# Optimization experiments

Measured on AMD Instinct MI355X. Metric: run time of the kernel, lower is better.

The kernel has to match this reference:

```python
import jax, jax.numpy as jnp
import numpy as np


def setup_inputs() -> dict:
    key = jax.random.key(0)
    B, C, H, W = 32, 128, 112, 112
    inp = jax.random.normal(key, (B, C, H, W), dtype=jnp.float32)
    # binomial blur filter for filt_size=4: outer([1,3,3,1]) normalized, repeated per channel
    a = np.array([1.0, 3.0, 3.0, 1.0])
    f = a[:, None] * a[None, :]
    f = f / f.sum()
    filt = jnp.asarray(np.broadcast_to(f[None, None], (C, 1, 4, 4)).copy(), dtype=jnp.float32)
    return {"inp": inp, "filt": filt}


def _polyphase_select_l2(x):
    # x: [B,C,H,W] with even H,W (aps_pad is a no-op). Returns [B] int index in {0..3}.
    p0 = x[:, :, 0::2, 0::2]
    p1 = x[:, :, 1::2, 0::2]
    p2 = x[:, :, 0::2, 1::2]
    p3 = x[:, :, 1::2, 1::2]
    norms = jnp.stack(
        [jnp.sqrt(jnp.sum(p * p, axis=(1, 2, 3))) for p in (p0, p1, p2, p3)], axis=1
    )  # [B,4]
    return jnp.argmax(norms, axis=1)


def reference(inp, filt):
    # 1) per-sample polyphase component selection on the raw input (criterion 'l2')
    idx = _polyphase_select_l2(inp)  # [B]
    C = inp.shape[1]
    # 2) reflect pad (left=1, right=2, top=1, bottom=2 for filt_size=4) + depthwise blur
    xp = jnp.pad(inp, ((0, 0), (0, 0), (1, 2), (1, 2)), mode='reflect')
    blurred = jax.lax.conv_general_dilated(
        xp, filt, window_strides=(1, 1), padding='VALID',
        dimension_numbers=('NCHW', 'OIHW', 'NCHW'), feature_group_count=C)
    # 3) stride-2 polyphase downsample selecting the chosen phase per sample
    p0 = blurred[:, :, 0::2, 0::2]
    p1 = blurred[:, :, 1::2, 0::2]
    p2 = blurred[:, :, 0::2, 1::2]
    p3 = blurred[:, :, 1::2, 1::2]
    poly = jnp.stack([p0, p1, p2, p3], axis=1)  # [B,4,C,H/2,W/2]
    out = jnp.take_along_axis(poly, idx[:, None, None, None, None], axis=1)[:, 0]
    return out  # [B,C,H/2,W/2]
```

## Files before the change

kernel.cpp:

```cpp
#include <hip/hip_runtime.h>

#define HW_    12544
#define W_     112
#define C_     128
#define OHW_   3136
#define OW_    56
#define NCHUNK 49

__global__ __launch_bounds__(512) void phase_norms(const float* __restrict__ inp,
                                                   float* __restrict__ part) {
    const int b = blockIdx.y;
    const float4* src = (const float4*)(inp + (size_t)b * (C_ * HW_));
    const unsigned tid = threadIdx.x;
    const unsigned base = blockIdx.x * 8192u + tid;

    float s[4] = {0.f, 0.f, 0.f, 0.f};
#pragma unroll
    for (int k = 0; k < 16; ++k) {
        unsigned g = base + k * 512u;
        float4 v = src[g];
        unsigned hp = (g / 28u) & 1u;
        s[hp]      += v.x * v.x + v.z * v.z;
        s[hp + 2u] += v.y * v.y + v.w * v.w;
    }

#pragma unroll
    for (int p = 0; p < 4; ++p) {
        float v = s[p];
        for (int off = 32; off > 0; off >>= 1) v += __shfl_down(v, off);
        s[p] = v;
    }

    __shared__ float bs[8][4];
    const unsigned wid = tid >> 6;
    if ((tid & 63u) == 0u) {
#pragma unroll
        for (int p = 0; p < 4; ++p) bs[wid][p] = s[p];
    }
    __syncthreads();
    if (tid < 4) {
        float v = 0.f;
#pragma unroll
        for (int w = 0; w < 8; ++w) v += bs[w][tid];
        part[((size_t)b * NCHUNK + blockIdx.x) * 4 + tid] = v;
    }
}

__global__ __launch_bounds__(128) void finalize_idx(const float* __restrict__ part,
                                                    int* __restrict__ pidx) {
    const int t = threadIdx.x;
    const int b = t >> 2, p = t & 3;
    float s = 0.f;
    for (int c = 0; c < NCHUNK; ++c) s += part[b * (NCHUNK * 4) + c * 4 + p];
    const int g = t & ~3;
    const float v0 = __shfl(s, g + 0), v1 = __shfl(s, g + 1);
    const float v2 = __shfl(s, g + 2), v3 = __shfl(s, g + 3);
    if (p == 0) {
        int idx = 0; float best = v0;
        if (v1 > best) { best = v1; idx = 1; }
        if (v2 > best) { best = v2; idx = 2; }
        if (v3 > best) { best = v3; idx = 3; }
        pidx[b] = idx;
    }
}

__global__ __launch_bounds__(256) void blur_select(const float* __restrict__ inp,
                                                   const int* __restrict__ pidx,
                                                   float* __restrict__ out) {
    __shared__ float h[59 * 56];
    const int blk = blockIdx.x;
    const int bc  = blk >> 1;
    const int oh0 = (blk & 1) * 28;
    const int t   = threadIdx.x;

    const int phase = pidx[bc >> 7];
    const int dr = phase & 1, dc = phase >> 1;
    const float* P = inp + (size_t)bc * HW_;
    const int jbase = 2 * oh0 - 1;

    for (int q = t; q < 59 * 5; q += 256) {
        const int rr = q / 5;
        const int s  = 1 + (q - 5 * rr);
        int j = jbase + rr;
        int aj = j < 0 ? -j : j;
        j = aj < 222 - aj ? aj : 222 - aj;
        const float4* rp = (const float4*)(P + j * W_) + (4 * s - 1);
        float4 va[6];
#pragma unroll
        for (int i = 0; i < 6; ++i) va[i] = rp[i];
        float xa[24];
#pragma unroll
        for (int i = 0; i < 6; ++i) {
            xa[4 * i + 0] = va[i].x; xa[4 * i + 1] = va[i].y;
            xa[4 * i + 2] = va[i].z; xa[4 * i + 3] = va[i].w;
        }
        float hh[8];
        if (dc == 0) {
#pragma unroll
            for (int u = 0; u < 8; ++u)
                hh[u] = (xa[2*u+3] + xa[2*u+6]) + 3.f * (xa[2*u+4] + xa[2*u+5]);
        } else {
#pragma unroll
            for (int u = 0; u < 8; ++u)
                hh[u] = (xa[2*u+4] + xa[2*u+7]) + 3.f * (xa[2*u+5] + xa[2*u+6]);
        }
        float* dst = &h[rr * 56 + 8 * s];
        *(float4*)dst       = make_float4(hh[0], hh[1], hh[2], hh[3]);
        *(float4*)(dst + 4) = make_float4(hh[4], hh[5], hh[6], hh[7]);
    }

    for (int rr = t; rr < 59; rr += 256) {
        int j = jbase + rr;
        int aj = j < 0 ? -j : j;
        j = aj < 222 - aj ? aj : 222 - aj;
        const float4* rp = (const float4*)(P + j * W_);
        float4 a4[5], b4[5];
#pragma unroll
        for (int i = 0; i < 5; ++i) { a4[i] = rp[i]; b4[i] = rp[23 + i]; }
        float xa[20], xb[22];
#pragma unroll
        for (int i = 0; i < 5; ++i) {
            xa[4*i+0] = a4[i].x; xa[4*i+1] = a4[i].y; xa[4*i+2] = a4[i].z; xa[4*i+3] = a4[i].w;
            xb[4*i+0] = b4[i].x; xb[4*i+1] = b4[i].y; xb[4*i+2] = b4[i].z; xb[4*i+3] = b4[i].w;
        }
        xb[20] = xb[18];
        xb[21] = xb[17];
        float hl[8], hr[8];
        if (dc == 0) {
            hl[0] = (xa[1] + xa[2]) + 3.f * (xa[0] + xa[1]);
#pragma unroll
            for (int u = 1; u < 8; ++u)
                hl[u] = (xa[2*u-1] + xa[2*u+2]) + 3.f * (xa[2*u] + xa[2*u+1]);
#pragma unroll
            for (int u = 0; u < 8; ++u)
                hr[u] = (xb[2*u+3] + xb[2*u+6]) + 3.f * (xb[2*u+4] + xb[2*u+5]);
        } else {
#pragma unroll
            for (int u = 0; u < 8; ++u)
                hl[u] = (xa[2*u] + xa[2*u+3]) + 3.f * (xa[2*u+1] + xa[2*u+2]);
#pragma unroll
            for (int u = 0; u < 8; ++u)
                hr[u] = (xb[2*u+4] + xb[2*u+7]) + 3.f * (xb[2*u+5] + xb[2*u+6]);
        }
        float* dl = &h[rr * 56];
        *(float4*)dl        = make_float4(hl[0], hl[1], hl[2], hl[3]);
        *(float4*)(dl + 4)  = make_float4(hl[4], hl[5], hl[6], hl[7]);
        *(float4*)(dl + 48) = make_float4(hr[0], hr[1], hr[2], hr[3]);
        *(float4*)(dl + 52) = make_float4(hr[4], hr[5], hr[6], hr[7]);
    }

    __syncthreads();

    float* o = out + (size_t)bc * OHW_ + oh0 * OW_;
    for (int v = t; v < 392; v += 256) {
        const int ohl = v / 14;
        const int q   = v - 14 * ohl;
        const float* hb = &h[(2 * ohl + dr) * 56 + 4 * q];
        const float4 h0 = *(const float4*)hb;
        const float4 h1 = *(const float4*)(hb + 56);
        const float4 h2 = *(const float4*)(hb + 112);
        const float4 h3 = *(const float4*)(hb + 168);
        float4 r;
        r.x = ((h0.x + h3.x) + 3.f * (h1.x + h2.x)) * 0.015625f;
        r.y = ((h0.y + h3.y) + 3.f * (h1.y + h2.y)) * 0.015625f;
        r.z = ((h0.z + h3.z) + 3.f * (h1.z + h2.z)) * 0.015625f;
        r.w = ((h0.w + h3.w) + 3.f * (h1.w + h2.w)) * 0.015625f;
        *(float4*)&o[ohl * 56 + 4 * q] = r;
    }
}

extern "C" void kernel_launch(void* const* d_in, const int* in_sizes, int n_in,
                              void* d_out, int out_size, void* d_ws, size_t ws_size,
                              hipStream_t stream) {
    const float* inp = (const float*)d_in[0];
    float* part = (float*)d_ws;
    int* pidx = (int*)((char*)d_ws + 32 * NCHUNK * 4 * sizeof(float));
    phase_norms<<<dim3(NCHUNK, 32), 512, 0, stream>>>(inp, part);
    finalize_idx<<<1, 128, 0, stream>>>(part, pidx);
    blur_select<<<8192, 256, 0, stream>>>(inp, pidx, (float*)d_out);
}
```

Before: 88.72 us.

## Compute blur outputs directly per thread without shared-memory staging

Replaces the shared-memory horizontal-pass staging in blur_select with a per-thread direct computation. Each thread reads four reflected input rows of 24 floats and produces 8 outputs, with no __syncthreads. It also computes only the rows needed for the selected row phase, rather than every row of the tile. This removes LDS traffic and the block barrier, at the cost of redundant global/L2 reads of overlapping input rows across threads. The grid is resized so each thread owns one 8-wide output segment.

```diff
diff --git a/kernel.cpp b/kernel.cpp
--- a/kernel.cpp
+++ b/kernel.cpp
@@ -23,14 +23,12 @@
         s[hp]      += v.x * v.x + v.z * v.z;
         s[hp + 2u] += v.y * v.y + v.w * v.w;
     }
-
 #pragma unroll
     for (int p = 0; p < 4; ++p) {
         float v = s[p];
         for (int off = 32; off > 0; off >>= 1) v += __shfl_down(v, off);
         s[p] = v;
     }
-
     __shared__ float bs[8][4];
     const unsigned wid = tid >> 6;
     if ((tid & 63u) == 0u) {
@@ -67,106 +65,75 @@
 __global__ __launch_bounds__(256) void blur_select(const float* __restrict__ inp,
                                                    const int* __restrict__ pidx,
                                                    float* __restrict__ out) {
-    __shared__ float h[59 * 56];
-    const int blk = blockIdx.x;
-    const int bc  = blk >> 1;
-    const int oh0 = (blk & 1) * 28;
-    const int t   = threadIdx.x;
+    const int g  = blockIdx.x * 256 + threadIdx.x;
+    const int bc = g / 392;
+    const int r  = g - bc * 392;
+    const int oh = r / 7;
+    const int s  = r - oh * 7;
+    const int ph = pidx[bc >> 7];
+    const int dr = ph & 1, dc = ph >> 1;
+    const float* P = inp + (size_t)bc * HW_;
 
-    const int phase = pidx[bc >> 7];
-    const int dr = phase & 1, dc = phase >> 1;
-    const float* P = inp + (size_t)bc * HW_;
-    const int jbase = 2 * oh0 - 1;
+    const int base4 = (s == 0) ? 0 : ((s == 6) ? 22 : 4 * s - 1);
+    const int jb = 2 * oh + dr - 1;
 
-    for (int q = t; q < 59 * 5; q += 256) {
-        const int rr = q / 5;
-        const int s  = 1 + (q - 5 * rr);
-        int j = jbase + rr;
+    float acc[8] = {0.f, 0.f, 0.f, 0.f, 0.f, 0.f, 0.f, 0.f};
+
+#pragma unroll
+    for (int k = 0; k < 4; ++k) {
+        int j = jb + k;
         int aj = j < 0 ? -j : j;
         j = aj < 222 - aj ? aj : 222 - aj;
-        const float4* rp = (const float4*)(P + j * W_) + (4 * s - 1);
-        float4 va[6];
+        const float4* rp = (const float4*)(P + j * W_) + base4;
+        const float4 v0 = rp[0], v1 = rp[1], v2 = rp[2];
+        const float4 v3 = rp[3], v4 = rp[4], v5 = rp[5];
+        float y[24] = {v0.x, v0.y, v0.z, v0.w, v1.x, v1.y, v1.z, v1.w,
+                       v2.x, v2.y, v2.z, v2.w, v3.x, v3.y, v3.z, v3.w,
+                       v4.x, v4.y, v4.z, v4.w, v5.x, v5.y, v5.z, v5.w};
+        float h[8];
+        if (s == 0) {
+            if (dc == 0) {
+                h[0] = 3.f * y[0] + 4.f * y[1] + y[2];
 #pragma unroll
-        for (int i = 0; i < 6; ++i) va[i] = rp[i];
-        float xa[24];
+                for (int u = 1; u < 8; ++u)
+                    h[u] = (y[2*u-1] + y[2*u+2]) + 3.f * (y[2*u] + y[2*u+1]);
+            } else {
 #pragma unroll
-        for (int i = 0; i < 6; ++i) {
-            xa[4 * i + 0] = va[i].x; xa[4 * i + 1] = va[i].y;
-            xa[4 * i + 2] = va[i].z; xa[4 * i + 3] = va[i].w;
+                for (int u = 0; u < 8; ++u)
+                    h[u] = (y[2*u] + y[2*u+3]) + 3.f * (y[2*u+1] + y[2*u+2]);
+            }
+        } else if (s == 6) {
+            if (dc == 0) {
+#pragma unroll
+                for (int u = 0; u < 7; ++u)
+                    h[u] = (y[2*u+7] + y[2*u+10]) + 3.f * (y[2*u+8] + y[2*u+9]);
+            } else {
+#pragma unroll
+                for (int u = 0; u < 7; ++u)
+                    h[u] = (y[2*u+8] + y[2*u+11]) + 3.f * (y[2*u+9] + y[2*u+10]);
+            }
+            h[7] = y[21] + 4.f * y[22] + 3.f * y[23];
+        } else {
+            if (dc == 0) {
+#pragma unroll
+                for (int u = 0; u < 8; ++u)
+                    h[u] = (y[2*u+3] + y[2*u+6]) + 3.f * (y[2*u+4] + y[2*u+5]);
+            } else {
+#pragma unroll
+                for (int u = 0; u < 8; ++u)
+                    h[u] = (y[2*u+4] + y[2*u+7]) + 3.f * (y[2*u+5] + y[2*u+6]);
+            }
         }
-        float hh[8];
-        if (dc == 0) {
+        const float wk = (k == 1 || k == 2) ? 3.f : 1.f;
 #pragma unroll
-            for (int u = 0; u < 8; ++u)
-                hh[u] = (xa[2*u+3] + xa[2*u+6]) + 3.f * (xa[2*u+4] + xa[2*u+5]);
-        } else {
-#pragma unroll
-            for (int u = 0; u < 8; ++u)
-                hh[u] = (xa[2*u+4] + xa[2*u+7]) + 3.f * (xa[2*u+5] + xa[2*u+6]);
-        }
-        float* dst = &h[rr * 56 + 8 * s];
-        *(float4*)dst       = make_float4(hh[0], hh[1], hh[2], hh[3]);
-        *(float4*)(dst + 4) = make_float4(hh[4], hh[5], hh[6], hh[7]);
+        for (int u = 0; u < 8; ++u) acc[u] += wk * h[u];
     }
 
-    for (int rr = t; rr < 59; rr += 256) {
-        int j = jbase + rr;
-        int aj = j < 0 ? -j : j;
-        j = aj < 222 - aj ? aj : 222 - aj;
-        const float4* rp = (const float4*)(P + j * W_);
-        float4 a4[5], b4[5];
-#pragma unroll
-        for (int i = 0; i < 5; ++i) { a4[i] = rp[i]; b4[i] = rp[23 + i]; }
-        float xa[20], xb[22];
-#pragma unroll
-        for (int i = 0; i < 5; ++i) {
-            xa[4*i+0] = a4[i].x; xa[4*i+1] = a4[i].y; xa[4*i+2] = a4[i].z; xa[4*i+3] = a4[i].w;
-            xb[4*i+0] = b4[i].x; xb[4*i+1] = b4[i].y; xb[4*i+2] = b4[i].z; xb[4*i+3] = b4[i].w;
-        }
-        xb[20] = xb[18];
-        xb[21] = xb[17];
-        float hl[8], hr[8];
-        if (dc == 0) {
-            hl[0] = (xa[1] + xa[2]) + 3.f * (xa[0] + xa[1]);
-#pragma unroll
-            for (int u = 1; u < 8; ++u)
-                hl[u] = (xa[2*u-1] + xa[2*u+2]) + 3.f * (xa[2*u] + xa[2*u+1]);
-#pragma unroll
-            for (int u = 0; u < 8; ++u)
-                hr[u] = (xb[2*u+3] + xb[2*u+6]) + 3.f * (xb[2*u+4] + xb[2*u+5]);
-        } else {
-#pragma unroll
-            for (int u = 0; u < 8; ++u)
-                hl[u] = (xa[2*u] + xa[2*u+3]) + 3.f * (xa[2*u+1] + xa[2*u+2]);
-#pragma unroll
-            for (int u = 0; u < 8; ++u)
-                hr[u] = (xb[2*u+4] + xb[2*u+7]) + 3.f * (xb[2*u+5] + xb[2*u+6]);
-        }
-        float* dl = &h[rr * 56];
-        *(float4*)dl        = make_float4(hl[0], hl[1], hl[2], hl[3]);
-        *(float4*)(dl + 4)  = make_float4(hl[4], hl[5], hl[6], hl[7]);
-        *(float4*)(dl + 48) = make_float4(hr[0], hr[1], hr[2], hr[3]);
-        *(float4*)(dl + 52) = make_float4(hr[4], hr[5], hr[6], hr[7]);
-    }
-
-    __syncthreads();
-
-    float* o = out + (size_t)bc * OHW_ + oh0 * OW_;
-    for (int v = t; v < 392; v += 256) {
-        const int ohl = v / 14;
-        const int q   = v - 14 * ohl;
-        const float* hb = &h[(2 * ohl + dr) * 56 + 4 * q];
-        const float4 h0 = *(const float4*)hb;
-        const float4 h1 = *(const float4*)(hb + 56);
-        const float4 h2 = *(const float4*)(hb + 112);
-        const float4 h3 = *(const float4*)(hb + 168);
-        float4 r;
-        r.x = ((h0.x + h3.x) + 3.f * (h1.x + h2.x)) * 0.015625f;
-        r.y = ((h0.y + h3.y) + 3.f * (h1.y + h2.y)) * 0.015625f;
-        r.z = ((h0.z + h3.z) + 3.f * (h1.z + h2.z)) * 0.015625f;
-        r.w = ((h0.w + h3.w) + 3.f * (h1.w + h2.w)) * 0.015625f;
-        *(float4*)&o[ohl * 56 + 4 * q] = r;
-    }
+    float* o = out + (size_t)bc * OHW_ + oh * OW_ + 8 * s;
+    *(float4*)o = make_float4(acc[0] * 0.015625f, acc[1] * 0.015625f,
+                              acc[2] * 0.015625f, acc[3] * 0.015625f);
+    *(float4*)(o + 4) = make_float4(acc[4] * 0.015625f, acc[5] * 0.015625f,
+                                    acc[6] * 0.015625f, acc[7] * 0.015625f);
 }
 
 extern "C" void kernel_launch(void* const* d_in, const int* in_sizes, int n_in,
@@ -177,5 +144,5 @@
     int* pidx = (int*)((char*)d_ws + 32 * NCHUNK * 4 * sizeof(float));
     phase_norms<<<dim3(NCHUNK, 32), 512, 0, stream>>>(inp, part);
     finalize_idx<<<1, 128, 0, stream>>>(part, pidx);
-    blur_select<<<8192, 256, 0, stream>>>(inp, pidx, (float*)d_out);
+    blur_select<<<6272, 256, 0, stream>>>(inp, pidx, (float*)d_out);
 }
```

New measurement: 111.0 us. 25.1% more time.
